# Performance work log

Hardware: AMD Instinct MI355X
Metric: run time of the kernel (lower is better)

## Reference

```python
import jax, jax.numpy as jnp
import numpy as np

N_TOKENS, MODEL_DIM, NUM_EXPERTS = 65536, 1024, 64
CAPACITY_FACTOR = 1.0


def setup_inputs() -> dict:
    key = jax.random.key(0)
    k1, k2 = jax.random.split(key)
    x = jax.random.normal(k1, (N_TOKENS, MODEL_DIM), dtype=jnp.float32)
    # gate projection weight, torch Linear stores [out_features, in_features]
    wg = jax.random.normal(k2, (NUM_EXPERTS, MODEL_DIM), dtype=jnp.float32) * (1.0 / np.sqrt(MODEL_DIM))
    return {"x": x, "wg": wg}


def reference(x, wg):
    N, E = x.shape[0], wg.shape[0]
    logits = x @ wg.T                              # [N, E]
    # training-branch capacity: capacity_factor * ceil(N / E)
    capacity = int(CAPACITY_FACTOR * ((N + E - 1) // E))
    indices1_s = jnp.argmax(logits, axis=1)        # [N] top-1 expert per token
    gates = jax.nn.softmax(logits, axis=1)         # [N, E]
    mask1 = jax.nn.one_hot(indices1_s, E, dtype=gates.dtype)  # [N, E]
    gates1_s = jnp.sum(gates * mask1, axis=1)      # [N] gate value of chosen expert
    # locations1_s[i] = number of earlier tokens routed to the same expert
    # (exclusive prefix count = inclusive cumsum - 1 at the selected column)
    locations1 = jnp.cumsum(mask1, axis=0) - 1.0   # [N, E]
    locations1_s = jnp.sum(locations1 * mask1, axis=1).astype(jnp.int32)
    # auxiliary load-balance loss (float32 branch of the original)
    me = jnp.sum(gates, axis=0)                    # [E]
    ce = jnp.sum(mask1, axis=0)                    # [E]
    l_aux = jnp.sum(me * ce) * (E / (N * N))
    return (l_aux, indices1_s.astype(jnp.int32), capacity, locations1_s, gates1_s, E)
```

## Files before the change

kernel.cpp:

```cpp
#include <hip/hip_runtime.h>

#define NT 65536
#define MD 1024
#define NE 64
#define TB 128
#define NGATE (NT / TB)

typedef short bf16x8 __attribute__((ext_vector_type(8)));
typedef float f32x4  __attribute__((ext_vector_type(4)));

__device__ __forceinline__ void split1(float f, ushort& h, ushort& m, ushort& lo) {
    unsigned u  = __float_as_uint(f);
    unsigned hb = u & 0xFFFF0000u;
    float    r1 = f - __uint_as_float(hb);
    unsigned mb = __float_as_uint(r1) & 0xFFFF0000u;
    float    r2 = r1 - __uint_as_float(mb);
    h  = (ushort)(hb >> 16);
    m  = (ushort)(mb >> 16);
    lo = (ushort)(__float_as_uint(r2) >> 16);
}

__device__ __forceinline__ void split8(const float4 a, const float4 b,
                                       bf16x8& h, bf16x8& m, bf16x8& lo) {
    float f[8] = {a.x, a.y, a.z, a.w, b.x, b.y, b.z, b.w};
#pragma unroll
    for (int j = 0; j < 8; ++j) {
        ushort hh, mm, ll;
        split1(f[j], hh, mm, ll);
        h[j] = (short)hh; m[j] = (short)mm; lo[j] = (short)ll;
    }
}

__global__ __launch_bounds__(256) void prep_kernel(
    const float* __restrict__ wg, ushort* __restrict__ wgp,
    float* __restrict__ me)
{
    const int idx = blockIdx.x * 256 + threadIdx.x;
    if (blockIdx.x == 0 && threadIdx.x < NE) me[threadIdx.x] = 0.f;
    const int l  = idx & 63;
    const int nt = (idx >> 6) & 3;
    const int c  = idx >> 8;
    const int e  = nt * 16 + (l & 15);
    const int k0 = c * 32 + (l >> 4) * 8;
    const float* src = wg + (size_t)e * MD + k0;
    float4 a = *(const float4*)(src);
    float4 b = *(const float4*)(src + 4);
    bf16x8 h, m, lo;
    split8(a, b, h, m, lo);
    *(bf16x8*)(wgp + (size_t)idx * 8)          = h;
    *(bf16x8*)(wgp + 65536 + (size_t)idx * 8)  = m;
    *(bf16x8*)(wgp + 131072 + (size_t)idx * 8) = lo;
}

#define MFMA6(accv, xh, xm, xl, wh, wm, wl)                                        \
    accv = __builtin_amdgcn_mfma_f32_16x16x32_bf16(xh, wh, accv, 0, 0, 0);         \
    accv = __builtin_amdgcn_mfma_f32_16x16x32_bf16(xh, wm, accv, 0, 0, 0);         \
    accv = __builtin_amdgcn_mfma_f32_16x16x32_bf16(xm, wh, accv, 0, 0, 0);         \
    accv = __builtin_amdgcn_mfma_f32_16x16x32_bf16(xm, wm, accv, 0, 0, 0);         \
    accv = __builtin_amdgcn_mfma_f32_16x16x32_bf16(xh, wl, accv, 0, 0, 0);         \
    accv = __builtin_amdgcn_mfma_f32_16x16x32_bf16(xl, wh, accv, 0, 0, 0);

#define LDB(dst_h, dst_m, dst_l, nt)                                               \
    dst_h = *(const bf16x8*)(pb + (nt) * 512);                                     \
    dst_m = *(const bf16x8*)(pb + 65536 + (nt) * 512);                             \
    dst_l = *(const bf16x8*)(pb + 131072 + (nt) * 512);

__global__ __launch_bounds__(512, 4) void gate_kernel(
    const float* __restrict__ x, const ushort* __restrict__ wgp,
    float* __restrict__ out, unsigned* __restrict__ packed_ws,
    int* __restrict__ hist_ws, float* __restrict__ me)
{
    __shared__ float lt[TB * 65];
    __shared__ float inv[TB];

    const int tid = threadIdx.x;
    const int wv  = tid >> 6;
    const int l   = tid & 63;
    const int g   = wv & 3;
    const int h   = wv >> 2;
    const int lr  = l & 15;
    const int lg  = l >> 4;

    const float* xa0 = x + (size_t)(blockIdx.x * TB + g * 32 + lr) * MD
                         + h * 512 + lg * 8;
    const float* xa1 = xa0 + 16 * MD;
    const ushort* wb = wgp + (size_t)l * 8 + (size_t)h * 16 * 2048;

    f32x4 acc[2][4];
#pragma unroll
    for (int mt = 0; mt < 2; ++mt)
#pragma unroll
        for (int nt = 0; nt < 4; ++nt) acc[mt][nt] = f32x4{0.f, 0.f, 0.f, 0.f};

    float4 a00 = *(const float4*)(xa0);
    float4 a01 = *(const float4*)(xa0 + 4);
    float4 a10 = *(const float4*)(xa1);
    float4 a11 = *(const float4*)(xa1 + 4);

    for (int c = 0; c < 16; ++c) {
        const ushort* pb = wb + c * 2048;
        bf16x8 ah0, am0, al0, ah1, am1, al1;
        split8(a00, a01, ah0, am0, al0);
        split8(a10, a11, ah1, am1, al1);
        if (c < 15) {
            const float* xn0 = xa0 + (c + 1) * 32;
            const float* xn1 = xa1 + (c + 1) * 32;
            a00 = *(const float4*)(xn0);
            a01 = *(const float4*)(xn0 + 4);
            a10 = *(const float4*)(xn1);
            a11 = *(const float4*)(xn1 + 4);
        }
        bf16x8 bhA, bmA, blA, bhB, bmB, blB;
        LDB(bhA, bmA, blA, 0);
        LDB(bhB, bmB, blB, 1);
        MFMA6(acc[0][0], ah0, am0, al0, bhA, bmA, blA);
        MFMA6(acc[1][0], ah1, am1, al1, bhA, bmA, blA);
        LDB(bhA, bmA, blA, 2);
        MFMA6(acc[0][1], ah0, am0, al0, bhB, bmB, blB);
        MFMA6(acc[1][1], ah1, am1, al1, bhB, bmB, blB);
        LDB(bhB, bmB, blB, 3);
        MFMA6(acc[0][2], ah0, am0, al0, bhA, bmA, blA);
        MFMA6(acc[1][2], ah1, am1, al1, bhA, bmA, blA);
        MFMA6(acc[0][3], ah0, am0, al0, bhB, bmB, blB);
        MFMA6(acc[1][3], ah1, am1, al1, bhB, bmB, blB);
    }

    if (h == 0) {
#pragma unroll
        for (int mt = 0; mt < 2; ++mt)
#pragma unroll
            for (int nt = 0; nt < 4; ++nt)
#pragma unroll
                for (int r = 0; r < 4; ++r)
                    lt[(g * 32 + mt * 16 + lg * 4 + r) * 65 + nt * 16 + lr] =
                        acc[mt][nt][r];
    }
    __syncthreads();
    if (h == 1) {
#pragma unroll
        for (int mt = 0; mt < 2; ++mt)
#pragma unroll
            for (int nt = 0; nt < 4; ++nt)
#pragma unroll
                for (int r = 0; r < 4; ++r)
                    lt[(g * 32 + mt * 16 + lg * 4 + r) * 65 + nt * 16 + lr] +=
                        acc[mt][nt][r];
    }
    __syncthreads();

    if (tid < 128) {
        const int grp = tid >> 6;
        const int t   = tid & 63;
        float* row = &lt[(grp * 64 + t) * 65];
        float mx = -1e30f; int am = 0;
        for (int e = 0; e < NE; ++e) {
            float v = row[e];
            if (v > mx) { mx = v; am = e; }
        }
        float s = 0.f;
        for (int e = 0; e < NE; ++e) {
            float ev = __expf(row[e] - mx);
            row[e] = ev;
            s += ev;
        }
        float gv = 1.0f / s;
        const int gt = blockIdx.x * TB + grp * 64 + t;
        out[1 + gt] = (float)am;
        out[2 + 2 * NT + gt] = gv;
        inv[grp * 64 + t] = gv;

        const unsigned long long below = (1ull << t) - 1ull;
        int rank = 0, mycnt = 0;
        for (int e = 0; e < NE; ++e) {
            unsigned long long msk = __ballot(am == e);
            if (t == e)  mycnt = (int)__popcll(msk);
            if (am == e) rank  = (int)__popcll(msk & below);
        }
        packed_ws[gt] = (unsigned)am | ((unsigned)rank << 8);
        hist_ws[(blockIdx.x * 2 + grp) * NE + t] = mycnt;
    }
    __syncthreads();

    if (tid < 128) {
        const int grp = tid >> 6;
        const int e   = tid & 63;
        const float* base = &lt[grp * 64 * 65];
        const float* iv   = &inv[grp * 64];
        float s = 0.f;
        for (int t = 0; t < 64; ++t) s += base[t * 65 + e] * iv[t];
        atomicAdd(&me[e], s);
    }
}

__global__ __launch_bounds__(256) void scan_kernel(
    int* __restrict__ hist_ws, float* __restrict__ ce)
{
    const int e = blockIdx.x;
    const int tid = threadIdx.x;
    const int lane = tid & 63, wave = tid >> 6;
    __shared__ int wtot[4];

    int h[4];
#pragma unroll
    for (int j = 0; j < 4; ++j) h[j] = hist_ws[(tid * 4 + j) * NE + e];
    int s = h[0] + h[1] + h[2] + h[3];

    int scan = s;
#pragma unroll
    for (int d = 1; d < 64; d <<= 1) {
        int o = __shfl_up(scan, d, 64);
        if (lane >= d) scan += o;
    }
    if (lane == 63) wtot[wave] = scan;
    __syncthreads();
    int wpre = 0;
#pragma unroll
    for (int w = 0; w < 4; ++w)
        if (w < wave) wpre += wtot[w];

    int run = wpre + scan - s;
#pragma unroll
    for (int j = 0; j < 4; ++j) {
        hist_ws[(tid * 4 + j) * NE + e] = run;
        run += h[j];
    }
    if (tid == 255) ce[e] = (float)run;
}

__global__ __launch_bounds__(256) void emit_kernel(
    const unsigned* __restrict__ packed_ws, const int* __restrict__ offs_ws,
    const float* __restrict__ me, const float* __restrict__ ce,
    float* __restrict__ out)
{
    const int i = blockIdx.x * 256 + threadIdx.x;
    const unsigned p = packed_ws[i];
    const int am = (int)(p & 63u);
    const int rank = (int)(p >> 8);
    const int b = i >> 6;
    out[2 + NT + i] = (float)(offs_ws[b * NE + am] + rank);

    if (blockIdx.x == 0 && threadIdx.x < 64) {
        float v = me[threadIdx.x] * ce[threadIdx.x];
#pragma unroll
        for (int d = 32; d > 0; d >>= 1) v += __shfl_down(v, d, 64);
        if (threadIdx.x == 0) {
            out[0] = v * (float)((double)NE / ((double)NT * (double)NT));
            out[1 + NT] = 1024.0f;
            out[2 + 3 * NT] = 64.0f;
        }
    }
}

extern "C" void kernel_launch(void* const* d_in, const int* in_sizes, int n_in,
                              void* d_out, int out_size, void* d_ws, size_t ws_size,
                              hipStream_t stream)
{
    const float* x  = (const float*)d_in[0];
    const float* wg = (const float*)d_in[1];
    float* out = (float*)d_out;

    unsigned* packed_ws = (unsigned*)d_ws;
    int*      hist_ws   = (int*)((char*)d_ws + 262144);
    float*    me        = (float*)((char*)d_ws + 524288);
    float*    ce        = (float*)((char*)d_ws + 524544);
    ushort*   wgp       = (ushort*)((char*)d_ws + 524800);

    prep_kernel<<<32, 256, 0, stream>>>(wg, wgp, me);
    gate_kernel<<<NGATE, 512, 0, stream>>>(x, wgp, out, packed_ws, hist_ws, me);
    scan_kernel<<<NE, 256, 0, stream>>>(hist_ws, ce);
    emit_kernel<<<NT / 256, 256, 0, stream>>>(packed_ws, hist_ws, me, ce, out);
}
```

Measured before the change: 399.7 us.

## Stage gate weight tiles through double-buffered LDS shared across waves

Each wave used to read the split bf16 weight fragments straight from global memory, so the four waves in each K-half loaded identical data. Now the block loads each K-step weight chunk into shared memory cooperatively (three float4 per thread), double-buffered, and all waves read B fragments from LDS. The shared buffer is reused later for the logits tile. This removes redundant global/L2 weight traffic but adds a barrier every K-step and more LDS usage, which may limit occupancy.

Measured after the change: 382.8 us. 1.04x faster.

```diff
diff --git a/kernel.cpp b/kernel.cpp
--- a/kernel.cpp
+++ b/kernel.cpp
@@ -60,18 +60,15 @@
     accv = __builtin_amdgcn_mfma_f32_16x16x32_bf16(xh, wl, accv, 0, 0, 0);         \
     accv = __builtin_amdgcn_mfma_f32_16x16x32_bf16(xl, wh, accv, 0, 0, 0);
 
-#define LDB(dst_h, dst_m, dst_l, nt)                                               \
-    dst_h = *(const bf16x8*)(pb + (nt) * 512);                                     \
-    dst_m = *(const bf16x8*)(pb + 65536 + (nt) * 512);                             \
-    dst_l = *(const bf16x8*)(pb + 131072 + (nt) * 512);
-
 __global__ __launch_bounds__(512, 4) void gate_kernel(
     const float* __restrict__ x, const ushort* __restrict__ wgp,
     float* __restrict__ out, unsigned* __restrict__ packed_ws,
     int* __restrict__ hist_ws, float* __restrict__ me)
 {
-    __shared__ float lt[TB * 65];
+    __shared__ __align__(16) float uni[12288];
     __shared__ float inv[TB];
+    ushort* bsm = (ushort*)uni;
+    float*  lt  = uni;
 
     const int tid = threadIdx.x;
     const int wv  = tid >> 6;
@@ -84,45 +81,71 @@
     const float* xa0 = x + (size_t)(blockIdx.x * TB + g * 32 + lr) * MD
                          + h * 512 + lg * 8;
     const float* xa1 = xa0 + 16 * MD;
-    const ushort* wb = wgp + (size_t)l * 8 + (size_t)h * 16 * 2048;
+
+    const int id0 = wv * 3;
+    const int h0 = id0 / 12,       f0 = id0 % 12;
+    const int h1 = (id0 + 1) / 12, f1 = (id0 + 1) % 12;
+    const int h2 = (id0 + 2) / 12, f2 = (id0 + 2) % 12;
+    const ushort* gs0 = wgp + (f0 >> 2) * 65536 + ((h0 * 16) * 4 + (f0 & 3)) * 512 + l * 8;
+    const ushort* gs1 = wgp + (f1 >> 2) * 65536 + ((h1 * 16) * 4 + (f1 & 3)) * 512 + l * 8;
+    const ushort* gs2 = wgp + (f2 >> 2) * 65536 + ((h2 * 16) * 4 + (f2 & 3)) * 512 + l * 8;
 
     f32x4 acc[2][4];
 #pragma unroll
     for (int mt = 0; mt < 2; ++mt)
 #pragma unroll
         for (int nt = 0; nt < 4; ++nt) acc[mt][nt] = f32x4{0.f, 0.f, 0.f, 0.f};
+
+    {
+        float4 v0 = *(const float4*)(gs0);
+        float4 v1 = *(const float4*)(gs1);
+        float4 v2 = *(const float4*)(gs2);
+        *(float4*)(bsm + ((0 * 2 + h0) * 12 + f0) * 512 + l * 8) = v0;
+        *(float4*)(bsm + ((0 * 2 + h1) * 12 + f1) * 512 + l * 8) = v1;
+        *(float4*)(bsm + ((0 * 2 + h2) * 12 + f2) * 512 + l * 8) = v2;
+    }
 
     float4 a00 = *(const float4*)(xa0);
     float4 a01 = *(const float4*)(xa0 + 4);
     float4 a10 = *(const float4*)(xa1);
     float4 a11 = *(const float4*)(xa1 + 4);
-
-    for (int c = 0; c < 16; ++c) {
-        const ushort* pb = wb + c * 2048;
+    __syncthreads();
+
+    for (int s = 0; s < 16; ++s) {
+        const int p = s & 1;
+        float4 sv0, sv1, sv2;
+        if (s < 15) {
+            sv0 = *(const float4*)(gs0 + (s + 1) * 2048);
+            sv1 = *(const float4*)(gs1 + (s + 1) * 2048);
+            sv2 = *(const float4*)(gs2 + (s + 1) * 2048);
+        }
         bf16x8 ah0, am0, al0, ah1, am1, al1;
         split8(a00, a01, ah0, am0, al0);
         split8(a10, a11, ah1, am1, al1);
-        if (c < 15) {
-            const float* xn0 = xa0 + (c + 1) * 32;
-            const float* xn1 = xa1 + (c + 1) * 32;
+        if (s < 15) {
+            const float* xn0 = xa0 + (s + 1) * 32;
+            const float* xn1 = xa1 + (s + 1) * 32;
             a00 = *(const float4*)(xn0);
             a01 = *(const float4*)(xn0 + 4);
             a10 = *(const float4*)(xn1);
             a11 = *(const float4*)(xn1 + 4);
         }
-        bf16x8 bhA, bmA, blA, bhB, bmB, blB;
-        LDB(bhA, bmA, blA, 0);
-        LDB(bhB, bmB, blB, 1);
-        MFMA6(acc[0][0], ah0, am0, al0, bhA, bmA, blA);
-        MFMA6(acc[1][0], ah1, am1, al1, bhA, bmA, blA);
-        LDB(bhA, bmA, blA, 2);
-        MFMA6(acc[0][1], ah0, am0, al0, bhB, bmB, blB);
-        MFMA6(acc[1][1], ah1, am1, al1, bhB, bmB, blB);
-        LDB(bhB, bmB, blB, 3);
-        MFMA6(acc[0][2], ah0, am0, al0, bhA, bmA, blA);
-        MFMA6(acc[1][2], ah1, am1, al1, bhA, bmA, blA);
-        MFMA6(acc[0][3], ah0, am0, al0, bhB, bmB, blB);
-        MFMA6(acc[1][3], ah1, am1, al1, bhB, bmB, blB);
+        const ushort* pb = bsm + (p * 2 + h) * 6144 + l * 8;
+#pragma unroll
+        for (int nt = 0; nt < 4; ++nt) {
+            bf16x8 bh = *(const bf16x8*)(pb + (0 + nt) * 512);
+            bf16x8 bm = *(const bf16x8*)(pb + (4 + nt) * 512);
+            bf16x8 bl = *(const bf16x8*)(pb + (8 + nt) * 512);
+            MFMA6(acc[0][nt], ah0, am0, al0, bh, bm, bl);
+            MFMA6(acc[1][nt], ah1, am1, al1, bh, bm, bl);
+        }
+        if (s < 15) {
+            const int q = p ^ 1;
+            *(float4*)(bsm + ((q * 2 + h0) * 12 + f0) * 512 + l * 8) = sv0;
+            *(float4*)(bsm + ((q * 2 + h1) * 12 + f1) * 512 + l * 8) = sv1;
+            *(float4*)(bsm + ((q * 2 + h2) * 12 + f2) * 512 + l * 8) = sv2;
+        }
+        __syncthreads();
     }
 
     if (h == 0) {
@@ -157,13 +180,13 @@
             float v = row[e];
             if (v > mx) { mx = v; am = e; }
         }
-        float s = 0.f;
+        float sum = 0.f;
         for (int e = 0; e < NE; ++e) {
             float ev = __expf(row[e] - mx);
             row[e] = ev;
-            s += ev;
-        }
-        float gv = 1.0f / s;
+            sum += ev;
+        }
+        float gv = 1.0f / sum;
         const int gt = blockIdx.x * TB + grp * 64 + t;
         out[1 + gt] = (float)am;
         out[2 + 2 * NT + gt] = gv;
```
